# Kernel tuning notes

Hardware: AMD Instinct MI355X
Metric: run time of the kernel (lower is better)

Reference implementation:

```python
import jax, jax.numpy as jnp
import numpy as np

B, C, N = 16, 128, 2048
M = 1024
NUM_BINS = 4
BOUND = [1.2, 1.0, 0.8]  # interior bin boundaries (num_bins-1 values)


def setup_inputs() -> dict:
    key = jax.random.key(0)
    k1, k2, k3, k4, k5 = jax.random.split(key, 5)
    s = 1.0 / np.sqrt(C)
    x = jax.random.normal(k1, (B, C, N), jnp.float32)
    Wq = jax.random.normal(k2, (C, C), jnp.float32) * s
    Wk = jax.random.normal(k3, (C, C), jnp.float32) * s
    Wv = jax.random.normal(k4, (C, C), jnp.float32) * s
    bin_tokens = jax.random.normal(k5, (1, C, NUM_BINS), jnp.float32) * s
    return {"x": x, "Wq": Wq, "Wk": Wk, "Wv": Wv, "bin_tokens": bin_tokens}


def _forward(x, Wq, Wk, Wv, bin_tokens):
    Bb, Cc, Nn = x.shape
    nb = bin_tokens.shape[-1]
    toks = jnp.broadcast_to(bin_tokens, (Bb, Cc, nb))
    x_tok = jnp.concatenate([x, toks], axis=2)            # (B,C,N+nb)
    # 1x1 convs (bias=False) == channel matmuls; single head (H=1)
    q = jnp.einsum('oc,bcn->bno', Wq, x)[:, None]         # (B,1,N,dq)
    k = jnp.einsum('oc,bcn->bon', Wk, x_tok)[:, None]     # (B,1,dk,N+nb)
    v = jnp.einsum('oc,bcn->bon', Wv, x_tok)[:, None]     # (B,1,dv,N+nb)
    scale = jnp.sqrt(jnp.asarray(q.shape[-1], jnp.float32))
    energy = jnp.einsum('bhnd,bhdm->bhnm', q, k) / scale  # (B,1,N,N+nb)
    attn = jax.nn.softmax(energy, axis=-1)
    attn_points = attn[..., :Nn]                          # (B,1,N,N)
    attn_bins_pre = energy[..., Nn:]                      # (B,1,N,nb) pre-softmax token scores
    # idx_mode == 'col_sum': attention score per point = column sum
    score = jnp.sum(attn_points, axis=-2)                 # (B,1,N)
    # static bin partition (dynamic_boundaries disabled)
    upper = jnp.asarray([np.inf] + BOUND, jnp.float32)
    lower = jnp.asarray(BOUND + [-np.inf], jnp.float32)
    mask = (score[..., None] < upper) & (score[..., None] >= lower)  # (B,1,N,nb)
    maskf = mask.astype(jnp.float32)
    # bin weights ('mean_relu'): masked mean of token attention, then relu
    counts = jnp.sum(maskf, axis=2)                       # (B,1,nb)
    w_pre = jnp.sum(attn_bins_pre * maskf, axis=2) / (counts + 1e-8)
    bin_w = jax.nn.relu(w_pre[:, 0])                      # (B,nb)
    max_pts = jnp.sum(mask[:, 0].astype(jnp.int32), axis=1)  # (B,nb)
    # points per bin: proportional allocation clipped to capacity, remainder
    # filled greedily in bin order (deterministic, capacity-respecting)
    p = bin_w / jnp.maximum(jnp.sum(bin_w, axis=1, keepdims=True), 1e-8)
    k0 = jnp.minimum(jnp.floor(p * M).astype(jnp.int32), max_pts)
    deficit = M - jnp.sum(k0, axis=1, keepdims=True)      # >= 0
    cap = max_pts - k0
    cum = jnp.cumsum(cap, axis=1) - cap                   # exclusive cumsum
    extra = jnp.clip(deficit - cum, 0, cap)
    k_bins = k0 + extra                                   # (B,nb), rows sum to M
    # top-k_bins per bin by attention score ('topk' sample mode)
    s = score[:, 0]                                       # (B,N)
    s_b = jnp.where(mask[:, 0], s[:, :, None], -jnp.inf)  # (B,N,nb)
    order = jnp.argsort(-s_b, axis=1)
    ranks = jnp.argsort(order, axis=1)                    # rank within each bin
    selected = mask[:, 0] & (ranks < k_bins[:, None, :])  # (B,N,nb)
    sel_any = jnp.any(selected, axis=-1)                  # (B,N), exactly M true
    _, idx = jax.lax.top_k(sel_any.astype(jnp.float32), M)  # (B,M)
    index_down = idx[:, None, :]                          # (B,H=1,M)
    # gather selected attention rows and aggregate values
    idx_e = jnp.broadcast_to(index_down[..., None], (Bb, 1, M, attn.shape[-1]))
    attn_down = jnp.take_along_axis(attn, idx_e, axis=2)  # (B,1,M,N+nb)
    v_down = jnp.einsum('bhmk,bhdk->bhmd', attn_down, v)  # (B,1,M,dv)
    x_ds = v_down.transpose(0, 2, 1, 3).reshape(Bb, M, -1).transpose(0, 2, 1)  # (B,C,M)
    return x_ds, index_down


def reference(x, Wq, Wk, Wv, bin_tokens):
    return _forward(x, Wq, Wk, Wv, bin_tokens)
```

## Files before the change

kernel.cpp:

```cpp
#include <hip/hip_runtime.h>

#define BB 16
#define CC 128
#define NN 2048
#define MM2 2052
#define VST 2056
#define XTR 2056
#define MM 1024

constexpr float RSQRT_C = 0.08838834764831845f;

typedef unsigned short u16;
typedef __attribute__((ext_vector_type(8))) short bf16x8;
typedef __attribute__((ext_vector_type(8))) _Float16 f16x8;
typedef __attribute__((ext_vector_type(4))) float f32x4;

__device__ inline u16 f2b_rn(float f) {
  unsigned u = __float_as_uint(f);
  unsigned r = u + 0x7fffu + ((u >> 16) & 1u);
  return (u16)(r >> 16);
}
__device__ inline float b2f(u16 h) { return __uint_as_float(((unsigned)h) << 16); }
__device__ inline u16 f2h(float f) {
  union { _Float16 h; u16 u; } cv; cv.h = (_Float16)f; return cv.u;
}

constexpr size_t SZ_Q  = (size_t)BB*NN*CC*2;
constexpr size_t SZ_K  = (size_t)BB*MM2*CC*2;
constexpr size_t SZ_V  = (size_t)BB*CC*VST*2;
constexpr size_t oQH = 0;
constexpr size_t oQL = oQH + SZ_Q;
constexpr size_t oKH = oQL + SZ_Q;
constexpr size_t oKL = oKH + SZ_K;
constexpr size_t oVF = oKL + SZ_K;
constexpr size_t oRS0 = oVF + SZ_V;
constexpr size_t oEB  = oRS0 + (size_t)2*BB*NN*4;
constexpr size_t oSC0 = oEB  + (size_t)BB*NN*16;
constexpr size_t oSCORE = oSC0 + (size_t)8*BB*NN*4;
constexpr size_t oBIN = oSCORE + (size_t)BB*NN*4;
constexpr size_t oKB  = oBIN + (size_t)BB*NN*4;
constexpr size_t oFL  = oKB  + 256;
constexpr size_t oIDX = oFL  + (size_t)BB*NN*4;
constexpr size_t oXH  = oIDX + (size_t)BB*MM*4;
constexpr size_t oXL  = oXH  + (size_t)BB*XTR*CC*2;
constexpr size_t oWH  = oXL  + (size_t)BB*XTR*CC*2;
constexpr size_t oWL  = oWH  + (size_t)3*CC*CC*2;
constexpr size_t oPU  = oXH;
constexpr size_t SZ_PU = (size_t)BB*NN*VST*2;
constexpr size_t oOP  = oPU + SZ_PU;

__global__ __launch_bounds__(256) void splitX_kernel(
    const float* __restrict__ x, const float* __restrict__ bt,
    u16* __restrict__ XH, u16* __restrict__ XL)
{
  const int t = threadIdx.x;
  const int b  = blockIdx.x / 33;
  const int nt = blockIdx.x % 33;
  if (nt == 32) {
    for (int i = t; i < 4*128; i += 256) {
      int j = i >> 7, c = i & 127;
      float v = bt[c*4 + j];
      u16 hb = f2b_rn(v);
      size_t oi = ((size_t)b*XTR + NN + j)*CC + c;
      XH[oi] = hb; XL[oi] = f2b_rn(v - b2f(hb));
    }
    return;
  }
  __shared__ float xs[128][65];
  const int n0 = nt*64;
  for (int i = t; i < 128*64; i += 256) {
    int c = i >> 6, n = i & 63;
    xs[c][n] = x[((size_t)b*CC + c)*NN + n0 + n];
  }
  __syncthreads();
  for (int i = t; i < 64*128; i += 256) {
    int m = i >> 7, c = i & 127;
    float v = xs[c][m];
    u16 hb = f2b_rn(v);
    size_t oi = ((size_t)b*XTR + n0 + m)*CC + c;
    XH[oi] = hb; XL[oi] = f2b_rn(v - b2f(hb));
  }
}

__global__ __launch_bounds__(256) void splitW_kernel(
    const float* __restrict__ Wq, const float* __restrict__ Wk, const float* __restrict__ Wv,
    u16* __restrict__ WH, u16* __restrict__ WL)
{
  int i = blockIdx.x*256 + threadIdx.x;
  int w = i >> 14, rest = i & 16383;
  const float* W = (w == 0) ? Wq : (w == 1) ? Wk : Wv;
  float v = W[rest];
  u16 hb = f2b_rn(v);
  WH[i] = hb; WL[i] = f2b_rn(v - b2f(hb));
}

__global__ __launch_bounds__(256) void projM_kernel(
    const u16* __restrict__ XH, const u16* __restrict__ XL,
    const u16* __restrict__ WHs, const u16* __restrict__ WLs,
    u16* __restrict__ QH, u16* __restrict__ QL,
    u16* __restrict__ KH, u16* __restrict__ KL,
    u16* __restrict__ VF)
{
  __shared__ u16 xsh[64*128], xsl[64*128];
  const int t = threadIdx.x;
  const int b  = blockIdx.x / 33;
  const int mt = blockIdx.x % 33;
  const int m0 = mt*64;
  const int wv = t >> 6, lane = t & 63;
  const int l15 = lane & 15, lhi = lane >> 4;

  {
    const int row0 = t >> 4, chunk = t & 15;
    #pragma unroll
    for (int ii=0; ii<4; ++ii) {
      int r = row0 + ii*16; int gm = m0 + r;
      int dst = r*256 + ((chunk*16) ^ ((r&7)<<4));
      uint4 vh = make_uint4(0,0,0,0), vl = make_uint4(0,0,0,0);
      if (gm < MM2) {
        size_t g = ((size_t)b*XTR + gm)*CC + chunk*8;
        vh = *(const uint4*)(XH + g);
        vl = *(const uint4*)(XL + g);
      }
      *(uint4*)((char*)xsh + dst) = vh;
      *(uint4*)((char*)xsl + dst) = vl;
    }
  }
  __syncthreads();

  for (int w = (m0 >= NN) ? 1 : 0; w < 2; ++w) {
    const u16* whp = WHs + (size_t)w*CC*CC;
    const u16* wlp = WLs + (size_t)w*CC*CC;
    u16* OH = w ? KH : QH;
    u16* OL = w ? KL : QL;
    const float scl = w ? 1.0f : RSQRT_C;
    const int mlim = w ? MM2 : NN;
    for (int osub = 0; osub < 2; ++osub) {
      const int ocol = wv*32 + osub*16;
      bf16x8 wbh[4], wbl[4];
      #pragma unroll
      for (int it=0; it<4; ++it) {
        size_t wi = (size_t)(ocol + l15)*CC + it*32 + lhi*8;
        wbh[it] = *(const bf16x8*)(whp + wi);
        wbl[it] = *(const bf16x8*)(wlp + wi);
      }
      for (int msub = 0; msub < 4; ++msub) {
        const int mrow = msub*16 + l15;
        f32x4 acc = {0.f,0.f,0.f,0.f};
        #pragma unroll
        for (int it=0; it<4; ++it) {
          int byt = mrow*256 + ((it*64 + lhi*16) ^ ((mrow&7)<<4));
          bf16x8 ah = *(const bf16x8*)((const char*)xsh + byt);
          bf16x8 al = *(const bf16x8*)((const char*)xsl + byt);
          acc = __builtin_amdgcn_mfma_f32_16x16x32_bf16(ah, wbh[it], acc, 0,0,0);
          acc = __builtin_amdgcn_mfma_f32_16x16x32_bf16(ah, wbl[it], acc, 0,0,0);
          acc = __builtin_amdgcn_mfma_f32_16x16x32_bf16(al, wbh[it], acc, 0,0,0);
        }
        #pragma unroll
        for (int r=0;r<4;++r) {
          int m = m0 + msub*16 + lhi*4 + r;
          if (m < mlim) {
            float vv = acc[r] * scl;
            u16 hb = f2b_rn(vv);
            size_t oi = w ? ((size_t)b*MM2 + m)*CC + ocol + l15
                          : ((size_t)b*NN  + m)*CC + ocol + l15;
            OH[oi] = hb;
            OL[oi] = f2b_rn(vv - b2f(hb));
          }
        }
      }
    }
  }

  {
    const u16* whp = WHs + (size_t)2*CC*CC;
    const u16* wlp = WLs + (size_t)2*CC*CC;
    for (int osub = 0; osub < 2; ++osub) {
      const int ocol = wv*32 + osub*16;
      bf16x8 wbh[4], wbl[4];
      #pragma unroll
      for (int it=0; it<4; ++it) {
        size_t wi = (size_t)(ocol + l15)*CC + it*32 + lhi*8;
        wbh[it] = *(const bf16x8*)(whp + wi);
        wbl[it] = *(const bf16x8*)(wlp + wi);
      }
      for (int msub = 0; msub < 4; ++msub) {
        const int mrow = msub*16 + l15;
        f32x4 acc = {0.f,0.f,0.f,0.f};
        #pragma unroll
        for (int it=0; it<4; ++it) {
          int byt = mrow*256 + ((it*64 + lhi*16) ^ ((mrow&7)<<4));
          bf16x8 ah = *(const bf16x8*)((const char*)xsh + byt);
          bf16x8 al = *(const bf16x8*)((const char*)xsl + byt);
          acc = __builtin_amdgcn_mfma_f32_16x16x32_bf16(wbh[it], ah, acc, 0,0,0);
          acc = __builtin_amdgcn_mfma_f32_16x16x32_bf16(wbh[it], al, acc, 0,0,0);
          acc = __builtin_amdgcn_mfma_f32_16x16x32_bf16(wbl[it], ah, acc, 0,0,0);
        }
        #pragma unroll
        for (int r=0;r<4;++r) {
          int o = ocol + lhi*4 + r;
          int m = m0 + msub*16 + l15;
          if (m < VST)
            VF[((size_t)b*CC + o)*VST + m] = f2h(acc[r]);
        }
      }
    }
  }
}

__global__ __launch_bounds__(256) void fusedE_kernel(
    const u16* __restrict__ QH, const u16* __restrict__ QL,
    const u16* __restrict__ KH, const u16* __restrict__ KL,
    float* __restrict__ rsumP, float* __restrict__ ebins, u16* __restrict__ PU)
{
  __shared__ u16 kh[64*128], kl[64*128];
  const int t = threadIdx.x;
  const int half = blockIdx.x & 1;
  const int rest = blockIdx.x >> 1;
  const int b = rest >> 5;
  const int n0 = (rest & 31) * 64;
  const int wv = t >> 6, lane = t & 63;
  const int l15 = lane & 15, lhi = lane >> 4;
  const int nw = n0 + wv*16;
  const int ktBeg = half ? 17 : 0;
  const int ktEnd = half ? 33 : 17;

  bf16x8 qh[4], ql[4];
  {
    const size_t rb = ((size_t)b*NN + nw + l15)*CC + lhi*8;
    #pragma unroll
    for (int it=0; it<4; ++it) {
      qh[it] = *(const bf16x8*)(QH + rb + it*32);
      ql[it] = *(const bf16x8*)(QL + rb + it*32);
    }
  }
  float runsum[4] = {0.f, 0.f, 0.f, 0.f};

  for (int kt = ktBeg; kt < ktEnd; ++kt) {
    const int m0 = kt*64;
    __syncthreads();
    {
      const int row0 = t >> 4, chunk = t & 15;
      #pragma unroll
      for (int ii=0; ii<4; ++ii) {
        int r = row0 + ii*16; int gm = m0 + r;
        int dst = r*256 + ((chunk*16) ^ ((r&7)<<4));
        uint4 vh = make_uint4(0,0,0,0), vl = make_uint4(0,0,0,0);
        if (gm < MM2) {
          size_t g = ((size_t)b*MM2 + gm)*CC + chunk*8;
          vh = *(const uint4*)(KH + g);
          vl = *(const uint4*)(KL + g);
        }
        *(uint4*)((char*)kh + dst) = vh;
        *(uint4*)((char*)kl + dst) = vl;
      }
    }
    __syncthreads();
    const int mcEnd = (kt == 32) ? 1 : 4;
    for (int mc = 0; mc < mcEnd; ++mc) {
      f32x4 acc = {0.f,0.f,0.f,0.f};
      const int mrow = mc*16 + l15;
      #pragma unroll
      for (int it=0; it<4; ++it) {
        int byt = mrow*256 + ((it*64 + lhi*16) ^ ((mrow&7)<<4));
        bf16x8 bh = *(const bf16x8*)((const char*)kh + byt);
        bf16x8 bl = *(const bf16x8*)((const char*)kl + byt);
        acc = __builtin_amdgcn_mfma_f32_16x16x32_bf16(qh[it], bh, acc, 0,0,0);
        acc = __builtin_amdgcn_mfma_f32_16x16x32_bf16(qh[it], bl, acc, 0,0,0);
        acc = __builtin_amdgcn_mfma_f32_16x16x32_bf16(ql[it], bh, acc, 0,0,0);
      }
      const int m = m0 + mrow;
      if (kt == 32 && l15 < 4) {
        #pragma unroll
        for (int r=0;r<4;++r)
          ebins[((size_t)b*NN + nw + lhi*4 + r)*4 + l15] = acc[r];
      }
      const bool valid = (m < MM2);
      #pragma unroll
      for (int r=0;r<4;++r) {
        float ex = valid ? __expf(acc[r]) : 0.f;
        if (m < VST)
          PU[((size_t)b*NN + nw + lhi*4 + r)*VST + m] = f2h(ex);
        runsum[r] += ex;
      }
    }
  }
  #pragma unroll
  for (int r=0;r<4;++r) {
    runsum[r] += __shfl_xor(runsum[r], 1);
    runsum[r] += __shfl_xor(runsum[r], 2);
    runsum[r] += __shfl_xor(runsum[r], 4);
    runsum[r] += __shfl_xor(runsum[r], 8);
  }
  if (l15 == 0) {
    float* rs = rsumP + (size_t)half*BB*NN;
    #pragma unroll
    for (int r=0;r<4;++r)
      rs[(size_t)b*NN + nw + lhi*4 + r] = runsum[r];
  }
}

__global__ __launch_bounds__(256) void colsum_kernel(
    const u16* __restrict__ PU, const float* __restrict__ rsumP,
    float* __restrict__ scoreP)
{
  __shared__ float sirs[256];
  const int t = threadIdx.x;
  const int blk = blockIdx.x;
  const int ns = blk & 7;
  const int mt = (blk >> 3) & 3;
  const int b  = blk >> 5;
  const int n0 = ns*256;
  const int m0 = mt*512;
  {
    size_t ri = (size_t)b*NN + n0 + t;
    sirs[t] = 1.0f / (rsumP[ri] + rsumP[(size_t)BB*NN + ri]);
  }
  __syncthreads();
  float s0a = 0.f, s1a = 0.f;
  const u16* base = PU + ((size_t)b*NN + n0)*VST + m0 + 2*t;
  #pragma unroll 4
  for (int n = 0; n < 256; ++n) {
    unsigned pv = *(const unsigned*)(base + (size_t)n*VST);
    union { unsigned u; _Float16 h[2]; } cv; cv.u = pv;
    float w = sirs[n];
    s0a = fmaf((float)cv.h[0], w, s0a);
    s1a = fmaf((float)cv.h[1], w, s1a);
  }
  float2 o; o.x = s0a; o.y = s1a;
  *(float2*)(scoreP + (size_t)ns*BB*NN + (size_t)b*NN + m0 + 2*t) = o;
}

__global__ __launch_bounds__(256) void bin_kernel(
    const float* __restrict__ scoreP, const float* __restrict__ ebins,
    float* __restrict__ score, int* __restrict__ binof, int* __restrict__ kbins)
{
  const int b = blockIdx.x, t = threadIdx.x;
  float wsm[4] = {0.f,0.f,0.f,0.f};
  int   cnt[4] = {0,0,0,0};
  for (int n = t; n < NN; n += 256) {
    size_t si = (size_t)b*NN + n;
    float s = 0.f;
    #pragma unroll
    for (int h = 0; h < 8; ++h) s += scoreP[(size_t)h*BB*NN + si];
    score[si] = s;
    int j = (s >= 1.2f) ? 0 : (s >= 1.0f) ? 1 : (s >= 0.8f) ? 2 : 3;
    binof[si] = j;
    wsm[j] += ebins[si*4 + j];
    cnt[j] += 1;
  }
  #pragma unroll
  for (int j=0;j<4;j++){
    for (int off=1; off<64; off<<=1){
      wsm[j] += __shfl_xor(wsm[j], off);
      cnt[j] += __shfl_xor(cnt[j], off);
    }
  }
  __shared__ float wred[4][4];
  __shared__ int   cred[4][4];
  int wave = t >> 6, lane = t & 63;
  if (lane == 0) for (int j=0;j<4;j++){ wred[wave][j]=wsm[j]; cred[wave][j]=cnt[j]; }
  __syncthreads();
  if (t == 0) {
    float wsum[4]; int cs[4];
    for (int j=0;j<4;j++){
      wsum[j]=wred[0][j]+wred[1][j]+wred[2][j]+wred[3][j];
      cs[j]=cred[0][j]+cred[1][j]+cred[2][j]+cred[3][j];
    }
    float bw[4]; float sbw = 0.f;
    for (int j=0;j<4;j++){
      float wp = wsum[j] / ((float)cs[j] + 1e-8f);
      bw[j] = fmaxf(wp, 0.f); sbw += bw[j];
    }
    float den = fmaxf(sbw, 1e-8f);
    int k0[4]; int sk0 = 0;
    for (int j=0;j<4;j++){
      float p = bw[j] / den;
      int kk = (int)floorf(p * 1024.0f);
      if (kk > cs[j]) kk = cs[j];
      k0[j]=kk; sk0 += kk;
    }
    int deficit = 1024 - sk0;
    int cum = 0;
    for (int j=0;j<4;j++){
      int cap = cs[j] - k0[j];
      int ex = deficit - cum; if (ex < 0) ex = 0; if (ex > cap) ex = cap;
      kbins[b*4+j] = k0[j] + ex;
      cum += cap;
    }
  }
}

__global__ __launch_bounds__(256) void topk_kernel(
    const float* __restrict__ score, const int* __restrict__ binof,
    const int* __restrict__ kbins, int* __restrict__ flags)
{
  __shared__ unsigned long long arr[2048];
  const int t = threadIdx.x;
  const int b = blockIdx.x >> 2;
  const int j = blockIdx.x & 3;
  for (int n = t; n < NN; n += 256) {
    unsigned long long comp = 0ull;
    if (binof[(size_t)b*NN+n] == j) {
      unsigned int bits = __float_as_uint(score[(size_t)b*NN+n]);
      bits = (bits & 0x80000000u) ? ~bits : (bits | 0x80000000u);
      comp = ((unsigned long long)bits << 32) |
             (unsigned long long)(0xFFFFFFFFu - (unsigned)n);
    }
    arr[n] = ~comp;
  }
  __syncthreads();
  for (int ksz = 2; ksz <= 2048; ksz <<= 1) {
    for (int jsz = ksz >> 1; jsz > 0; jsz >>= 1) {
      for (int i = t; i < 2048; i += 256) {
        int ixj = i ^ jsz;
        if (ixj > i) {
          unsigned long long a = arr[i], bv = arr[ixj];
          bool up = ((i & ksz) == 0);
          if ((a > bv) == up) { arr[i] = bv; arr[ixj] = a; }
        }
      }
      __syncthreads();
    }
  }
  const int kb = kbins[b*4+j];
  for (int i = t; i < kb; i += 256) {
    unsigned long long comp = ~arr[i];
    int n = (int)(0xFFFFFFFFu - (unsigned)(comp & 0xFFFFFFFFull));
    flags[(size_t)b*NN + n] = 1;
  }
}

__global__ __launch_bounds__(256) void scan_kernel(
    const int* __restrict__ flags, int* __restrict__ idxl, float* __restrict__ outIdx)
{
  __shared__ int tsum[256];
  const int b = blockIdx.x, t = threadIdx.x;
  int f[8]; int c8 = 0;
  const int base = t * 8;
  #pragma unroll
  for (int i=0;i<8;i++){ f[i] = flags[(size_t)b*NN + base + i]; c8 += f[i]; }
  tsum[t] = c8;
  __syncthreads();
  for (int off=1; off<256; off<<=1) {
    int v = (t >= off) ? tsum[t-off] : 0;
    __syncthreads();
    tsum[t] += v;
    __syncthreads();
  }
  int pos = tsum[t] - c8;
  #pragma unroll
  for (int i=0;i<8;i++){
    if (f[i] && pos < MM) {
      idxl[(size_t)b*MM + pos] = base + i;
      outIdx[(size_t)b*MM + pos] = (float)(base + i);
      pos++;
    }
  }
}

__global__ __launch_bounds__(256) void outC_kernel(
    const u16* __restrict__ PU, const u16* __restrict__ VF,
    const float* __restrict__ rsumP,
    const int* __restrict__ idxl, float* __restrict__ oPart)
{
  __shared__ u16 psh[64*64];
  __shared__ u16 vsh[128*64];
  __shared__ int rid[64];
  __shared__ float ssel[64];
  const int t = threadIdx.x;
  const int third = blockIdx.x % 3;
  const int rest  = blockIdx.x / 3;
  const int b  = rest >> 4;
  const int s0 = (rest & 15) * 64;
  const int wv = t >> 6, lane = t & 63;
  const int l15 = lane & 15, lhi = lane >> 4;
  const int ktBeg = third * 11, ktEnd = ktBeg + 11;

  if (t < 64) {
    int n = idxl[(size_t)b*MM + s0 + t];
    rid[t] = n;
    size_t ri = (size_t)b*NN + n;
    ssel[t] = 1.0f / (rsumP[ri] + rsumP[(size_t)BB*NN + ri]);
  }

  f32x4 oacc[8];
  #pragma unroll
  for (int ct=0; ct<8; ++ct) oacc[ct] = (f32x4){0.f,0.f,0.f,0.f};

  for (int kt = ktBeg; kt < ktEnd; ++kt) {
    const int m0 = kt*64;
    __syncthreads();
    #pragma unroll
    for (int ii=0; ii<2; ++ii) {
      int item = t + 256*ii;
      int row = item >> 3, ch = item & 7;
      int gm = m0 + ch*8;
      uint4 v = make_uint4(0,0,0,0);
      if (gm < VST) v = *(const uint4*)(PU + ((size_t)b*NN + rid[row])*VST + gm);
      *(uint4*)((char*)psh + row*128 + ((ch*16) ^ ((row&7)<<4))) = v;
    }
    #pragma unroll
    for (int ii=0; ii<4; ++ii) {
      int item = t + 256*ii;
      int c = item >> 3, ch = item & 7;
      int gm = m0 + ch*8;
      uint4 v = make_uint4(0,0,0,0);
      if (gm < VST) v = *(const uint4*)(VF + ((size_t)b*CC + c)*VST + gm);
      *(uint4*)((char*)vsh + c*128 + ((ch*16) ^ ((c&7)<<4))) = v;
    }
    __syncthreads();
    #pragma unroll
    for (int ki=0; ki<2; ++ki) {
      const int prow = wv*16 + l15;
      f16x8 pa = *(const f16x8*)((const char*)psh + prow*128 + ((ki*64 + lhi*16) ^ ((prow&7)<<4)));
      #pragma unroll
      for (int ct=0; ct<8; ++ct) {
        int c = ct*16 + l15;
        f16x8 vb = *(const f16x8*)((const char*)vsh + c*128 + ((ki*64 + lhi*16) ^ ((c&7)<<4)));
        oacc[ct] = __builtin_amdgcn_mfma_f32_16x16x32_f16(pa, vb, oacc[ct], 0,0,0);
      }
    }
  }
  float* op = oPart + (size_t)third*BB*CC*MM;
  #pragma unroll
  for (int ct=0; ct<8; ++ct) {
    #pragma unroll
    for (int r=0;r<4;++r) {
      op[((size_t)b*CC + ct*16 + l15)*MM + s0 + wv*16 + lhi*4 + r] =
          oacc[ct][r] * ssel[wv*16 + lhi*4 + r];
    }
  }
}

__global__ __launch_bounds__(256) void merge_kernel(
    const float* __restrict__ oPart, float* __restrict__ out0)
{
  const size_t i = ((size_t)blockIdx.x*256 + threadIdx.x)*4;
  const float4 a = *(const float4*)(oPart + i);
  const float4 b = *(const float4*)(oPart + (size_t)BB*CC*MM + i);
  const float4 c = *(const float4*)(oPart + (size_t)2*BB*CC*MM + i);
  float4 o;
  o.x = a.x + b.x + c.x;
  o.y = a.y + b.y + c.y;
  o.z = a.z + b.z + c.z;
  o.w = a.w + b.w + c.w;
  *(float4*)(out0 + i) = o;
}

extern "C" void kernel_launch(void* const* d_in, const int* in_sizes, int n_in,
                              void* d_out, int out_size, void* d_ws, size_t ws_size,
                              hipStream_t stream) {
  const float* x  = (const float*)d_in[0];
  const float* Wq = (const float*)d_in[1];
  const float* Wk = (const float*)d_in[2];
  const float* Wv = (const float*)d_in[3];
  const float* bt = (const float*)d_in[4];
  float* out = (float*)d_out;
  char* ws = (char*)d_ws;

  u16* QH = (u16*)(ws + oQH);
  u16* QL = (u16*)(ws + oQL);
  u16* KH = (u16*)(ws + oKH);
  u16* KL = (u16*)(ws + oKL);
  u16* VF = (u16*)(ws + oVF);
  float* rsumP = (float*)(ws + oRS0);
  float* ebins = (float*)(ws + oEB);
  float* scoreP= (float*)(ws + oSC0);
  float* score = (float*)(ws + oSCORE);
  int* binof = (int*)(ws + oBIN);
  int* kbins = (int*)(ws + oKB);
  int* flags = (int*)(ws + oFL);
  int* idxl  = (int*)(ws + oIDX);
  u16* XH = (u16*)(ws + oXH);
  u16* XL = (u16*)(ws + oXL);
  u16* WHs = (u16*)(ws + oWH);
  u16* WLs = (u16*)(ws + oWL);
  u16* PU  = (u16*)(ws + oPU);
  float* oPart = (float*)(ws + oOP);

  float* out0   = out;
  float* outIdx = out + (size_t)BB*CC*MM;

  (void)hipMemsetAsync(flags, 0, (size_t)BB*NN*sizeof(int), stream);

  hipLaunchKernelGGL(splitX_kernel,  dim3(528),  dim3(256), 0, stream, x, bt, XH, XL);
  hipLaunchKernelGGL(splitW_kernel,  dim3(192),  dim3(256), 0, stream, Wq, Wk, Wv, WHs, WLs);
  hipLaunchKernelGGL(projM_kernel,   dim3(528),  dim3(256), 0, stream, XH, XL, WHs, WLs, QH, QL, KH, KL, VF);
  hipLaunchKernelGGL(fusedE_kernel,  dim3(1024), dim3(256), 0, stream, QH, QL, KH, KL, rsumP, ebins, PU);
  hipLaunchKernelGGL(colsum_kernel,  dim3(512),  dim3(256), 0, stream, PU, rsumP, scoreP);
  hipLaunchKernelGGL(bin_kernel,     dim3(16),   dim3(256), 0, stream, scoreP, ebins, score, binof, kbins);
  hipLaunchKernelGGL(topk_kernel,    dim3(64),   dim3(256), 0, stream, score, binof, kbins, flags);
  hipLaunchKernelGGL(scan_kernel,    dim3(16),   dim3(256), 0, stream, flags, idxl, outIdx);
  hipLaunchKernelGGL(outC_kernel,    dim3(768),  dim3(256), 0, stream, PU, VF, rsumP, idxl, oPart);
  hipLaunchKernelGGL(merge_kernel,   dim3(2048), dim3(256), 0, stream, oPart, out0);
}
```

Before: 325.2 us.

## Fuse x bf16 split into projection kernel and specialize energy loop tail

Removes the separate splitX kernel: projM now loads x (and bin tokens) from global fp32, transposes through shared memory, and does the bf16 hi/lo split itself before the MFMA projection. This drops a full write and re-read of the split X buffers and one kernel launch. It also peels the final key tile (bin tokens) out of the fusedE main loop, so the main loop runs without the bound checks and ebins branch and writes through precomputed row pointers. The cost is extra shared memory in projM (an fp32 staging tile), which may lower occupancy.

Result: faster. 318.4 us (-2.1%).

```diff
diff --git a/kernel.cpp b/kernel.cpp
--- a/kernel.cpp
+++ b/kernel.cpp
@@ -5,7 +5,6 @@
 #define NN 2048
 #define MM2 2052
 #define VST 2056
-#define XTR 2056
 #define MM 1024
 
 constexpr float RSQRT_C = 0.08838834764831845f;
@@ -23,6 +22,14 @@
 __device__ inline float b2f(u16 h) { return __uint_as_float(((unsigned)h) << 16); }
 __device__ inline u16 f2h(float f) {
   union { _Float16 h; u16 u; } cv; cv.h = (_Float16)f; return cv.u;
+}
+__device__ inline void store8(u16* dst, const u16 h[8]) {
+  uint4 v;
+  v.x = (unsigned)h[0] | ((unsigned)h[1] << 16);
+  v.y = (unsigned)h[2] | ((unsigned)h[3] << 16);
+  v.z = (unsigned)h[4] | ((unsigned)h[5] << 16);
+  v.w = (unsigned)h[6] | ((unsigned)h[7] << 16);
+  *(uint4*)dst = v;
 }
 
 constexpr size_t SZ_Q  = (size_t)BB*NN*CC*2;
@@ -41,46 +48,11 @@
 constexpr size_t oKB  = oBIN + (size_t)BB*NN*4;
 constexpr size_t oFL  = oKB  + 256;
 constexpr size_t oIDX = oFL  + (size_t)BB*NN*4;
-constexpr size_t oXH  = oIDX + (size_t)BB*MM*4;
-constexpr size_t oXL  = oXH  + (size_t)BB*XTR*CC*2;
-constexpr size_t oWH  = oXL  + (size_t)BB*XTR*CC*2;
+constexpr size_t oWH  = oIDX + (size_t)BB*MM*4;
 constexpr size_t oWL  = oWH  + (size_t)3*CC*CC*2;
-constexpr size_t oPU  = oXH;
+constexpr size_t oPU  = oWL  + (size_t)3*CC*CC*2;
 constexpr size_t SZ_PU = (size_t)BB*NN*VST*2;
 constexpr size_t oOP  = oPU + SZ_PU;
-
-__global__ __launch_bounds__(256) void splitX_kernel(
-    const float* __restrict__ x, const float* __restrict__ bt,
-    u16* __restrict__ XH, u16* __restrict__ XL)
-{
-  const int t = threadIdx.x;
-  const int b  = blockIdx.x / 33;
-  const int nt = blockIdx.x % 33;
-  if (nt == 32) {
-    for (int i = t; i < 4*128; i += 256) {
-      int j = i >> 7, c = i & 127;
-      float v = bt[c*4 + j];
-      u16 hb = f2b_rn(v);
-      size_t oi = ((size_t)b*XTR + NN + j)*CC + c;
-      XH[oi] = hb; XL[oi] = f2b_rn(v - b2f(hb));
-    }
-    return;
-  }
-  __shared__ float xs[128][65];
-  const int n0 = nt*64;
-  for (int i = t; i < 128*64; i += 256) {
-    int c = i >> 6, n = i & 63;
-    xs[c][n] = x[((size_t)b*CC + c)*NN + n0 + n];
-  }
-  __syncthreads();
-  for (int i = t; i < 64*128; i += 256) {
-    int m = i >> 7, c = i & 127;
-    float v = xs[c][m];
-    u16 hb = f2b_rn(v);
-    size_t oi = ((size_t)b*XTR + n0 + m)*CC + c;
-    XH[oi] = hb; XL[oi] = f2b_rn(v - b2f(hb));
-  }
-}
 
 __global__ __launch_bounds__(256) void splitW_kernel(
     const float* __restrict__ Wq, const float* __restrict__ Wk, const float* __restrict__ Wv,
@@ -95,12 +67,13 @@
 }
 
 __global__ __launch_bounds__(256) void projM_kernel(
-    const u16* __restrict__ XH, const u16* __restrict__ XL,
+    const float* __restrict__ x, const float* __restrict__ bt,
     const u16* __restrict__ WHs, const u16* __restrict__ WLs,
     u16* __restrict__ QH, u16* __restrict__ QL,
     u16* __restrict__ KH, u16* __restrict__ KL,
     u16* __restrict__ VF)
 {
+  __shared__ float xs[64][130];
   __shared__ u16 xsh[64*128], xsl[64*128];
   const int t = threadIdx.x;
   const int b  = blockIdx.x / 33;
@@ -109,20 +82,34 @@
   const int wv = t >> 6, lane = t & 63;
   const int l15 = lane & 15, lhi = lane >> 4;
 
+  if (mt < 32) {
+    for (int i = t; i < 128*64; i += 256) {
+      int c = i >> 6, n = i & 63;
+      xs[n][c] = x[((size_t)b*CC + c)*NN + m0 + n];
+    }
+  } else {
+    for (int i = t; i < 64*128; i += 256) {
+      int n = i >> 7, c = i & 127;
+      xs[n][c] = (n < 4) ? bt[c*4 + n] : 0.f;
+    }
+  }
+  __syncthreads();
   {
     const int row0 = t >> 4, chunk = t & 15;
     #pragma unroll
     for (int ii=0; ii<4; ++ii) {
-      int r = row0 + ii*16; int gm = m0 + r;
+      int r = row0 + ii*16;
+      const float* src = &xs[r][chunk*8];
+      u16 hs[8], ls[8];
+      #pragma unroll
+      for (int j=0;j<8;++j) {
+        float v = src[j];
+        u16 hb = f2b_rn(v);
+        hs[j] = hb; ls[j] = f2b_rn(v - b2f(hb));
+      }
       int dst = r*256 + ((chunk*16) ^ ((r&7)<<4));
-      uint4 vh = make_uint4(0,0,0,0), vl = make_uint4(0,0,0,0);
-      if (gm < MM2) {
-        size_t g = ((size_t)b*XTR + gm)*CC + chunk*8;
-        vh = *(const uint4*)(XH + g);
-        vl = *(const uint4*)(XL + g);
-      }
-      *(uint4*)((char*)xsh + dst) = vh;
-      *(uint4*)((char*)xsl + dst) = vl;
+      store8((u16*)((char*)xsh + dst), hs);
+      store8((u16*)((char*)xsl + dst), ls);
     }
   }
   __syncthreads();
@@ -140,8 +127,8 @@
       #pragma unroll
       for (int it=0; it<4; ++it) {
         size_t wi = (size_t)(ocol + l15)*CC + it*32 + lhi*8;
-        wbh[it] = *(const bf16x8*)(whp + wi);
-        wbl[it] = *(const bf16x8*)(wlp + wi);
+        wbh[it] = *(const bf16x8*)(WHs + (size_t)w*CC*CC + wi);
+        wbl[it] = *(const bf16x8*)(WLs + (size_t)w*CC*CC + wi);
       }
       for (int msub = 0; msub < 4; ++msub) {
         const int mrow = msub*16 + l15;
@@ -169,6 +156,7 @@
         }
       }
     }
+    (void)whp; (void)wlp;
   }
 
   {
@@ -222,7 +210,7 @@
   const int l15 = lane & 15, lhi = lane >> 4;
   const int nw = n0 + wv*16;
   const int ktBeg = half ? 17 : 0;
-  const int ktEnd = half ? 33 : 17;
+  const int ktFastEnd = half ? 32 : 17;
 
   bf16x8 qh[4], ql[4];
   {
@@ -233,10 +221,52 @@
       ql[it] = *(const bf16x8*)(QL + rb + it*32);
     }
   }
+  u16* puR[4];
+  #pragma unroll
+  for (int r=0;r<4;++r)
+    puR[r] = PU + ((size_t)b*NN + nw + lhi*4 + r)*VST;
+
   float runsum[4] = {0.f, 0.f, 0.f, 0.f};
 
-  for (int kt = ktBeg; kt < ktEnd; ++kt) {
+  for (int kt = ktBeg; kt < ktFastEnd; ++kt) {
     const int m0 = kt*64;
+    __syncthreads();
+    {
+      const int row0 = t >> 4, chunk = t & 15;
+      #pragma unroll
+      for (int ii=0; ii<4; ++ii) {
+        int r = row0 + ii*16;
+        int dst = r*256 + ((chunk*16) ^ ((r&7)<<4));
+        size_t g = ((size_t)b*MM2 + m0 + r)*CC + chunk*8;
+        *(uint4*)((char*)kh + dst) = *(const uint4*)(KH + g);
+        *(uint4*)((char*)kl + dst) = *(const uint4*)(KL + g);
+      }
+    }
+    __syncthreads();
+    for (int mc = 0; mc < 4; ++mc) {
+      f32x4 acc = {0.f,0.f,0.f,0.f};
+      const int mrow = mc*16 + l15;
+      #pragma unroll
+      for (int it=0; it<4; ++it) {
+        int byt = mrow*256 + ((it*64 + lhi*16) ^ ((mrow&7)<<4));
+        bf16x8 bh = *(const bf16x8*)((const char*)kh + byt);
+        bf16x8 bl = *(const bf16x8*)((const char*)kl + byt);
+        acc = __builtin_amdgcn_mfma_f32_16x16x32_bf16(qh[it], bh, acc, 0,0,0);
+        acc = __builtin_amdgcn_mfma_f32_16x16x32_bf16(qh[it], bl, acc, 0,0,0);
+        acc = __builtin_amdgcn_mfma_f32_16x16x32_bf16(ql[it], bh, acc, 0,0,0);
+      }
+      const int m = m0 + mrow;
+      #pragma unroll
+      for (int r=0;r<4;++r) {
+        float ex = __expf(acc[r]);
+        puR[r][m] = f2h(ex);
+        runsum[r] += ex;
+      }
+    }
+  }
+
+  if (half) {
+    const int m0 = 2048;
     __syncthreads();
     {
       const int row0 = t >> 4, chunk = t & 15;
@@ -255,10 +285,9 @@
       }
     }
     __syncthreads();
-    const int mcEnd = (kt == 32) ? 1 : 4;
-    for (int mc = 0; mc < mcEnd; ++mc) {
+    {
       f32x4 acc = {0.f,0.f,0.f,0.f};
-      const int mrow = mc*16 + l15;
+      const int mrow = l15;
       #pragma unroll
       for (int it=0; it<4; ++it) {
         int byt = mrow*256 + ((it*64 + lhi*16) ^ ((mrow&7)<<4));
@@ -269,7 +298,7 @@
         acc = __builtin_amdgcn_mfma_f32_16x16x32_bf16(ql[it], bh, acc, 0,0,0);
       }
       const int m = m0 + mrow;
-      if (kt == 32 && l15 < 4) {
+      if (l15 < 4) {
         #pragma unroll
         for (int r=0;r<4;++r)
           ebins[((size_t)b*NN + nw + lhi*4 + r)*4 + l15] = acc[r];
@@ -278,12 +307,12 @@
       #pragma unroll
       for (int r=0;r<4;++r) {
         float ex = valid ? __expf(acc[r]) : 0.f;
-        if (m < VST)
-          PU[((size_t)b*NN + nw + lhi*4 + r)*VST + m] = f2h(ex);
+        if (m < VST) puR[r][m] = f2h(ex);
         runsum[r] += ex;
       }
     }
   }
+
   #pragma unroll
   for (int r=0;r<4;++r) {
     runsum[r] += __shfl_xor(runsum[r], 1);
@@ -571,8 +600,6 @@
   int* kbins = (int*)(ws + oKB);
   int* flags = (int*)(ws + oFL);
   int* idxl  = (int*)(ws + oIDX);
-  u16* XH = (u16*)(ws + oXH);
-  u16* XL = (u16*)(ws + oXL);
   u16* WHs = (u16*)(ws + oWH);
   u16* WLs = (u16*)(ws + oWL);
   u16* PU  = (u16*)(ws + oPU);
@@ -583,9 +610,8 @@
 
   (void)hipMemsetAsync(flags, 0, (size_t)BB*NN*sizeof(int), stream);
 
-  hipLaunchKernelGGL(splitX_kernel,  dim3(528),  dim3(256), 0, stream, x, bt, XH, XL);
   hipLaunchKernelGGL(splitW_kernel,  dim3(192),  dim3(256), 0, stream, Wq, Wk, Wv, WHs, WLs);
-  hipLaunchKernelGGL(projM_kernel,   dim3(528),  dim3(256), 0, stream, XH, XL, WHs, WLs, QH, QL, KH, KL, VF);
+  hipLaunchKernelGGL(projM_kernel,   dim3(528),  dim3(256), 0, stream, x, bt, WHs, WLs, QH, QL, KH, KL, VF);
   hipLaunchKernelGGL(fusedE_kernel,  dim3(1024), dim3(256), 0, stream, QH, QL, KH, KL, rsumP, ebins, PU);
   hipLaunchKernelGGL(colsum_kernel,  dim3(512),  dim3(256), 0, stream, PU, rsumP, scoreP);
   hipLaunchKernelGGL(bin_kernel,     dim3(16),   dim3(256), 0, stream, scoreP, ebins, score, binof, kbins);
```
